# Performance work log

Measured on AMD Instinct MI355X. Metric: run time of the kernel, lower is better.

Reference implementation:

```python
import jax, jax.numpy as jnp
import numpy as np
from math import factorial, sqrt, pi

LMAX, NSH = 2, 9
F = 64
N_RBF = 20
N_INTER = 2
N_ATOMS = 1000
N_PAIRS = 10000
CUTOFF = 5.0

# ---------- Clebsch-Gordan coefficients for real spherical harmonics ----------

def _cg_complex(l1, m1, l2, m2, l3, m3):
    # <l1 m1 l2 m2 | l3 m3> via Racah formula
    if m3 != m1 + m2 or not (abs(l1 - l2) <= l3 <= l1 + l2):
        return 0.0
    f = factorial
    pre = sqrt((2 * l3 + 1) * f(l3 + l1 - l2) * f(l3 - l1 + l2) * f(l1 + l2 - l3) / f(l1 + l2 + l3 + 1))
    pre *= sqrt(f(l3 + m3) * f(l3 - m3) * f(l1 - m1) * f(l1 + m1) * f(l2 - m2) * f(l2 + m2))
    s = 0.0
    for k in range(l1 + l2 - l3 + 1):
        d = [k, l1 + l2 - l3 - k, l1 - m1 - k, l2 + m2 - k, l3 - l2 + m1 + k, l3 - l1 - m2 + k]
        if min(d) < 0:
            continue
        s += (-1) ** k / np.prod([float(f(t)) for t in d])
    return pre * s

def _sh_indices(lmax):
    l = np.concatenate([np.full(2 * ll + 1, ll) for ll in range(lmax + 1)])
    m = np.concatenate([np.arange(-ll, ll + 1) for ll in range(lmax + 1)])
    return l, m

def _real_cg(lmax):
    lidx, midx = _sh_indices(lmax)
    n = (lmax + 1) ** 2
    cgc = np.zeros((n, n, n))
    for a in range(n):
        for b in range(n):
            for c in range(n):
                cgc[a, b, c] = _cg_complex(lidx[a], midx[a], lidx[b], midx[b], lidx[c], midx[c])
    # complex -> real spherical harmonic change of basis (per degree l)
    U = np.zeros((n, n), dtype=np.complex128)
    for ll in range(lmax + 1):
        base = ll * ll + ll
        U[base, base] = 1.0
        for m in range(1, ll + 1):
            U[base + m, base - m] = 1 / sqrt(2)
            U[base + m, base + m] = (-1) ** m / sqrt(2)
            U[base - m, base - m] = 1j / sqrt(2)
            U[base - m, base + m] = -1j * (-1) ** m / sqrt(2)
    cgr = np.einsum('ijk,ai,bj,ck->abc', cgc.astype(np.complex128), U, U, U.conj())
    parity = (-1.0) ** lidx
    mask = (parity[:, None, None] * parity[None, :, None]) == parity[None, None, :]
    cgr = np.real(cgr) * mask
    cgr = np.transpose(cgr, (2, 0, 1))  # [s_out, s_in(x), s_filter(Y)]
    s1, s2, s3 = np.nonzero(np.abs(cgr) > 1e-9)
    return s1, s2, s3, cgr[s1, s2, s3].astype(np.float32), lidx

_S1, _S2, _S3, _CGV, _LIDX = _real_cg(LMAX)
IDX1 = jnp.asarray(_S1)            # output sh channel per CG path
IDX2 = jnp.asarray(_S2)            # input-feature sh channel per CG path
IDX3 = jnp.asarray(_S3)            # Ylm sh channel per CG path
CGVAL = jnp.asarray(_CGV)          # CG value per path
WIDX = jnp.asarray(_LIDX[_S3])     # radial-filter degree per CG path
LIDX = jnp.asarray(_LIDX)          # degree of each of the 9 sh channels

# ---------- real spherical harmonics (lmax=2, orthonormal, m=-l..l order) ----------

def _rsh(u):
    x, y, z = u[:, 0], u[:, 1], u[:, 2]
    c1 = sqrt(3.0 / (4.0 * pi))
    c2 = 0.5 * sqrt(15.0 / pi)
    return jnp.stack([
        jnp.full_like(x, 0.5 / sqrt(pi)),
        c1 * y, c1 * z, c1 * x,
        c2 * x * y,
        c2 * y * z,
        0.25 * sqrt(5.0 / pi) * (3.0 * z * z - 1.0),
        c2 * x * z,
        0.25 * sqrt(15.0 / pi) * (x * x - y * y),
    ], axis=1)


def setup_inputs() -> dict:
    key = jax.random.key(0)
    ks = jax.random.split(key, 10)
    atomic_numbers = jax.random.randint(ks[0], (N_ATOMS,), 0, 100)
    r_ij = 1.5 * jax.random.normal(ks[1], (N_PAIRS, 3), dtype=jnp.float32)
    idx_i = jnp.sort(jax.random.randint(ks[2], (N_PAIRS,), 0, N_ATOMS))
    idx_j = jax.random.randint(ks[3], (N_PAIRS,), 0, N_ATOMS)
    emb = jax.random.normal(ks[4], (100, F), dtype=jnp.float32)
    def s(k, sh, fan):
        return jax.random.normal(k, sh, dtype=jnp.float32) / float(np.sqrt(fan))
    Wf = s(ks[5], (N_INTER, N_RBF, (LMAX + 1) * F), N_RBF)
    bf = jnp.zeros((N_INTER, (LMAX + 1) * F), jnp.float32)
    W1 = s(ks[6], (N_INTER, F, F), F)
    W2 = s(ks[7], (N_INTER, F, F), F)
    W3 = s(ks[8], (N_INTER, F, F), F)
    Wg = s(ks[9], (N_INTER, F, (LMAX + 1) * F), F)
    bg = jnp.zeros((N_INTER, (LMAX + 1) * F), jnp.float32)
    return dict(atomic_numbers=atomic_numbers, r_ij=r_ij, idx_i=idx_i, idx_j=idx_j,
                emb=emb, Wf=Wf, bf=bf, W1=W1, W2=W2, W3=W3, Wg=Wg, bg=bg)


def reference(atomic_numbers, r_ij, idx_i, idx_j, emb, Wf, bf, W1, W2, W3, Wg, bg):
    n_atoms = atomic_numbers.shape[0]
    d = jnp.linalg.norm(r_ij, axis=1, keepdims=True)          # [P,1]
    Yij = _rsh(r_ij / d)                                       # [P,9]
    offsets = jnp.linspace(0.0, CUTOFF, N_RBF)                 # GaussianRBF
    width = CUTOFF / (N_RBF - 1)
    radial = jnp.exp((-0.5 / (width * width)) * (d - offsets) ** 2)   # [P,n_rbf]
    cut = 0.5 * (jnp.cos(d * (pi / CUTOFF)) + 1.0) * (d < CUTOFF)     # [P,1]
    # nuclear embedding + scalar2rsh (zero-pad l>0 channels)
    x = jnp.zeros((n_atoms, NSH, F), emb.dtype).at[:, 0, :].set(emb[atomic_numbers])
    for t in range(N_INTER):
        # SO3Convolution
        Wij = (radial @ Wf[t] + bf[t]).reshape(-1, LMAX + 1, F) * cut[:, :, None]  # [P,lmax+1,F]
        xj = x[idx_j]                                                              # [P,9,F]
        v = xj[:, IDX2] * Yij[:, IDX3, None] * Wij[:, WIDX] * CGVAL[None, :, None]  # [P,nnz,F]
        yij = jnp.zeros_like(xj).at[:, IDX1].add(v)                                 # CG scatter
        dx = jax.ops.segment_sum(yij, idx_i, num_segments=n_atoms)                  # edge->node scatter
        # mixing1 + SO3TensorProduct
        ddx = dx @ W1[t]
        tp = jnp.zeros_like(dx).at[:, IDX1].add(dx[:, IDX2] * ddx[:, IDX3] * CGVAL[None, :, None])
        dx = (dx + tp) @ W2[t]
        # SO3ParametricGatedNonlinearity (gate from l=0 channel)
        gate = (dx[:, 0] @ Wg[t] + bg[t]).reshape(-1, LMAX + 1, F)
        dx = dx * jax.nn.sigmoid(gate[:, LIDX])
        dx = dx @ W3[t]
        x = x + dx
    return x  # multipole_representation [n_atoms, 9, F]; x[:,0] is scalar_representation
```

## Files before the change

kernel.cpp:

```cpp
#include <hip/hip_runtime.h>
#include <cmath>

constexpr int kNsh    = 9;
constexpr int kF      = 64;
constexpr int kNrbf   = 20;
constexpr int kNAtoms = 1000;
constexpr int kNPairs = 10000;
constexpr float kCutoffF = 5.0f;
constexpr int kMaxNZ  = 200;
constexpr int kCp     = 12;
constexpr int kXs     = kF * kCp;

struct CGSparse {
  int n;
  int c[kMaxNZ];
  int a[kMaxNZ];
  int b[kMaxNZ];
  float v[kMaxNZ];
};

constexpr double cfact(int n) {
  double r = 1.0;
  for (int i = 2; i <= n; i++) r *= (double)i;
  return r;
}
constexpr double cabs_(double x) { return x < 0 ? -x : x; }
constexpr double csqrt_(double x) {
  if (x <= 0.0) return 0.0;
  double g = x < 1.0 ? 1.0 : x;
  for (int i = 0; i < 60; i++) g = 0.5 * (g + x / g);
  return g;
}

constexpr double cg_cplx(int l1, int m1, int l2, int m2, int l3, int m3) {
  if (m3 != m1 + m2) return 0.0;
  int lo = l1 > l2 ? l1 - l2 : l2 - l1;
  if (l3 < lo || l3 > l1 + l2) return 0.0;
  double pre = csqrt_((2 * l3 + 1) * cfact(l3 + l1 - l2) * cfact(l3 - l1 + l2) *
                      cfact(l1 + l2 - l3) / cfact(l1 + l2 + l3 + 1));
  pre *= csqrt_(cfact(l3 + m3) * cfact(l3 - m3) * cfact(l1 - m1) *
                cfact(l1 + m1) * cfact(l2 - m2) * cfact(l2 + m2));
  double s = 0.0;
  for (int k = 0; k <= l1 + l2 - l3; k++) {
    int d0 = k, d1 = l1 + l2 - l3 - k, d2 = l1 - m1 - k;
    int d3 = l2 + m2 - k, d4 = l3 - l2 + m1 + k, d5 = l3 - l1 - m2 + k;
    if (d0 < 0 || d1 < 0 || d2 < 0 || d3 < 0 || d4 < 0 || d5 < 0) continue;
    double den = cfact(d0) * cfact(d1) * cfact(d2) * cfact(d3) * cfact(d4) * cfact(d5);
    s += ((k % 2) ? -1.0 : 1.0) / den;
  }
  return pre * s;
}

constexpr CGSparse build_cg() {
  CGSparse out{};
  int lidx[9] = {0, 1, 1, 1, 2, 2, 2, 2, 2};
  int midx[9] = {0, -1, 0, 1, -2, -1, 0, 1, 2};
  double Ur[9][9] = {};
  double Ui[9][9] = {};
  for (int l = 0; l <= 2; l++) {
    int base = l * l + l;
    Ur[base][base] = 1.0;
    for (int m = 1; m <= l; m++) {
      double s2 = 1.0 / csqrt_(2.0);
      double sgn = (m % 2) ? -1.0 : 1.0;
      Ur[base + m][base - m] = s2;
      Ur[base + m][base + m] = sgn * s2;
      Ui[base - m][base - m] = s2;
      Ui[base - m][base + m] = -sgn * s2;
    }
  }
  double cgr[9][9][9] = {};
  for (int i = 0; i < 9; i++)
    for (int j = 0; j < 9; j++)
      for (int k = 0; k < 9; k++) {
        double cv = cg_cplx(lidx[i], midx[i], lidx[j], midx[j], lidx[k], midx[k]);
        if (cv == 0.0) continue;
        for (int a2 = 0; a2 < 9; a2++) {
          if (Ur[a2][i] == 0.0 && Ui[a2][i] == 0.0) continue;
          for (int b2 = 0; b2 < 9; b2++) {
            if (Ur[b2][j] == 0.0 && Ui[b2][j] == 0.0) continue;
            for (int c2 = 0; c2 < 9; c2++) {
              if (Ur[c2][k] == 0.0 && Ui[c2][k] == 0.0) continue;
              double ar = Ur[a2][i], ai = Ui[a2][i];
              double br = Ur[b2][j], bi = Ui[b2][j];
              double cr = Ur[c2][k], ci = -Ui[c2][k];
              double pr = ar * br - ai * bi;
              double pi = ar * bi + ai * br;
              double rr = pr * cr - pi * ci;
              cgr[c2][a2][b2] += rr * cv;
            }
          }
        }
      }
  int n = 0;
  for (int c2 = 0; c2 < 9; c2++)
    for (int a2 = 0; a2 < 9; a2++)
      for (int b2 = 0; b2 < 9; b2++) {
        bool mask = ((lidx[a2] + lidx[b2]) % 2) == (lidx[c2] % 2);
        double v = mask ? cgr[c2][a2][b2] : 0.0;
        if (cabs_(v) > 1e-9) {
          out.c[n] = c2;
          out.a[n] = a2;
          out.b[n] = b2;
          out.v[n] = (float)v;
          n++;
        }
      }
  out.n = n;
  return out;
}

constexpr CGSparse CG = build_cg();
static_assert(CG.n > 0 && CG.n <= kMaxNZ, "CG table size out of range");

constexpr int kPreBlkPairs = kNPairs / 4;
constexpr int kPreBlkSeg   = (kNAtoms + 1 + 255) / 256;
constexpr int kPreBlkTotal = kPreBlkPairs + kPreBlkSeg;

__global__ __launch_bounds__(256) void k_pre(
    const float* __restrict__ rij, const float* __restrict__ Wf,
    const float* __restrict__ bf, const int* __restrict__ idx_i,
    float* __restrict__ Ypd, float* __restrict__ Wpair,
    int* __restrict__ seg) {
  const int blk = blockIdx.x;
  if (blk < kPreBlkPairs) {
    int wv = threadIdx.x >> 6;
    int f = threadIdx.x & 63;
    int p = blk * 4 + wv;
    float rx = rij[3 * p + 0], ry = rij[3 * p + 1], rz = rij[3 * p + 2];
    float d = sqrtf(rx * rx + ry * ry + rz * rz);
    float inv = 1.0f / d;
    float x = rx * inv, y = ry * inv, z = rz * inv;
    const float c0 = 0.28209479177387814f;
    const float c1 = 0.4886025119029199f;
    const float c2 = 1.0925484305920792f;
    const float c3 = 0.31539156525252005f;
    const float c4 = 0.5462742152960396f;
    if (f < 9) {
      float yv =
          (f == 0) ? c0 :
          (f == 1) ? c1 * y :
          (f == 2) ? c1 * z :
          (f == 3) ? c1 * x :
          (f == 4) ? c2 * x * y :
          (f == 5) ? c2 * y * z :
          (f == 6) ? c3 * (3.0f * z * z - 1.0f) :
          (f == 7) ? c2 * x * z :
                     c4 * (x * x - y * y);
      Ypd[p * 16 + f] = yv;
    }
    float cut = (d < kCutoffF) ? 0.5f * (cosf(d * (float)(M_PI / 5.0)) + 1.0f) : 0.0f;
    float radial[kNrbf];
    const float width = kCutoffF / (kNrbf - 1);
    const float coef = -0.5f / (width * width);
    #pragma unroll
    for (int k = 0; k < kNrbf; k++) {
      float off = (kCutoffF * k) / (kNrbf - 1);
      float tt = d - off;
      radial[k] = expf(coef * tt * tt);
    }
    #pragma unroll
    for (int t = 0; t < 2; t++) {
      #pragma unroll
      for (int l = 0; l < 3; l++) {
        float w = bf[t * 192 + l * 64 + f];
        #pragma unroll
        for (int k = 0; k < kNrbf; k++) {
          w += radial[k] * Wf[t * (kNrbf * 192) + k * 192 + l * 64 + f];
        }
        Wpair[t * (kNPairs * 192) + p * 192 + l * 64 + f] = w * cut;
      }
    }
  } else {
    int a = (blk - kPreBlkPairs) * 256 + threadIdx.x;
    if (a <= kNAtoms) {
      int lo = 0, hi = kNPairs;
      while (lo < hi) {
        int mid = (lo + hi) >> 1;
        if (idx_i[mid] < a) lo = mid + 1; else hi = mid;
      }
      seg[a] = lo;
    }
  }
}

__device__ __forceinline__ void stage_w(const float* __restrict__ W,
                                        float* __restrict__ sW, int tid) {
  const float4* g4 = (const float4*)W;
  float4* s4 = (float4*)sW;
  #pragma unroll
  for (int r = 0; r < 4; r++) s4[r * 256 + tid] = g4[r * 256 + tid];
}

__device__ __forceinline__ void mm_phase(const float* __restrict__ sA,
                                         const float* __restrict__ sW,
                                         float* __restrict__ sRw,
                                         int k0, int cgi, int fb) {
  if (cgi >= 3) return;
  const int c0 = cgi * 4;
  float acc[4][4];
  #pragma unroll
  for (int i = 0; i < 4; i++)
    #pragma unroll
    for (int j = 0; j < 4; j++) acc[i][j] = 0.f;
  #pragma unroll 4
  for (int kk = 0; kk < 16; kk++) {
    int k = k0 + kk;
    float4 av = *(const float4*)(sA + k * kCp + c0);
    float4 wv = *(const float4*)(sW + k * kF + fb);
    float a[4] = {av.x, av.y, av.z, av.w};
    float w[4] = {wv.x, wv.y, wv.z, wv.w};
    #pragma unroll
    for (int i = 0; i < 4; i++)
      #pragma unroll
      for (int j = 0; j < 4; j++) acc[i][j] += a[i] * w[j];
  }
  #pragma unroll
  for (int j = 0; j < 4; j++) {
    float4 v = {acc[0][j], acc[1][j], acc[2][j], acc[3][j]};
    *(float4*)(sRw + (fb + j) * kCp + c0) = v;
  }
}

template <int T>
__global__ __launch_bounds__(256) void k_inter(
    const float* __restrict__ Ypd, const float* __restrict__ Wpt,
    const int* __restrict__ seg, const int* __restrict__ idx_j,
    const int* __restrict__ Z, const float* __restrict__ emb,
    const float* __restrict__ x_in, const float* __restrict__ W1,
    const float* __restrict__ W2, const float* __restrict__ W3,
    const float* __restrict__ Wg, const float* __restrict__ bg,
    float* __restrict__ x_out) {
  const int atom = blockIdx.x;
  const int tid = threadIdx.x;
  const int wv = tid >> 6;
  const int lane = tid & 63;
  const int cgi = lane >> 4;
  const int fb = (lane & 15) * 4;
  const int k0 = wv * 16;

  __shared__ __align__(16) float sA[kF * kCp];
  __shared__ __align__(16) float sW[kF * kF];
  __shared__ __align__(16) float sR[4][kF * kCp];
  __shared__ __align__(16) float sGp[4][192];

  stage_w(W1, sW, tid);

  {
    float y[12];
    #pragma unroll
    for (int c = 0; c < 12; c++) y[c] = 0.f;
    const int s0 = seg[atom], s1 = seg[atom + 1];
    for (int p0 = s0 + wv; p0 < s1; p0 += 4) {
      const int p = __builtin_amdgcn_readfirstlane(p0);
      const int j = __builtin_amdgcn_readfirstlane(idx_j[p]);
      const float* Wp = Wpt + p * 192;
      float Wl0 = Wp[lane], Wl1 = Wp[64 + lane], Wl2 = Wp[128 + lane];
      const float* Yp = Ypd + p * 16;
      float YW[9];
      YW[0] = Yp[0] * Wl0;
      YW[1] = Yp[1] * Wl1;
      YW[2] = Yp[2] * Wl1;
      YW[3] = Yp[3] * Wl1;
      #pragma unroll
      for (int b = 4; b < 9; b++) YW[b] = Yp[b] * Wl2;
      if (T == 0) {
        float e = emb[Z[j] * kF + lane];
        #pragma unroll
        for (int q = 0; q < CG.n; q++) {
          if (CG.a[q] == 0) y[CG.c[q]] += CG.v[q] * YW[CG.b[q]] * e;
        }
      } else {
        const float* xj = x_in + j * kXs + lane * kCp;
        float xv[12];
        *(float4*)&xv[0] = *(const float4*)(xj + 0);
        *(float4*)&xv[4] = *(const float4*)(xj + 4);
        *(float4*)&xv[8] = *(const float4*)(xj + 8);
        #pragma unroll
        for (int q = 0; q < CG.n; q++) {
          y[CG.c[q]] += CG.v[q] * YW[CG.b[q]] * xv[CG.a[q]];
        }
      }
    }
    float4* r4 = (float4*)(sR[wv] + lane * kCp);
    r4[0] = *(float4*)&y[0];
    r4[1] = *(float4*)&y[4];
    r4[2] = *(float4*)&y[8];
  }
  __syncthreads();
  {
    const int i = tid * 3;
    #pragma unroll
    for (int d = 0; d < 3; d++) {
      sA[i + d] = sR[0][i + d] + sR[1][i + d] + sR[2][i + d] + sR[3][i + d];
    }
  }
  __syncthreads();

  mm_phase(sA, sW, sR[wv], k0, cgi, fb);
  __syncthreads();

  stage_w(W2, sW, tid);
  if (wv == 0) {
    float dxv[12], ddx[12];
    {
      const float4* sa = (const float4*)(sA + lane * kCp);
      *(float4*)&dxv[0] = sa[0];
      *(float4*)&dxv[4] = sa[1];
      *(float4*)&dxv[8] = sa[2];
    }
    #pragma unroll
    for (int c = 0; c < 12; c++) {
      ddx[c] = sR[0][lane * kCp + c] + sR[1][lane * kCp + c] +
               sR[2][lane * kCp + c] + sR[3][lane * kCp + c];
    }
    float t2[12];
    #pragma unroll
    for (int c = 0; c < 9; c++) t2[c] = dxv[c];
    t2[9] = 0.f; t2[10] = 0.f; t2[11] = 0.f;
    #pragma unroll
    for (int q = 0; q < CG.n; q++) {
      t2[CG.c[q]] += CG.v[q] * dxv[CG.a[q]] * ddx[CG.b[q]];
    }
    float4* sa = (float4*)(sA + lane * kCp);
    sa[0] = *(float4*)&t2[0];
    sa[1] = *(float4*)&t2[4];
    sa[2] = *(float4*)&t2[8];
  }
  __syncthreads();

  mm_phase(sA, sW, sR[wv], k0, cgi, fb);
  __syncthreads();

  stage_w(W3, sW, tid);
  {
    float g0 = 0.f, g1 = 0.f, g2 = 0.f;
    #pragma unroll 4
    for (int kk = 0; kk < 16; kk++) {
      int k = k0 + kk;
      float a = sR[0][k * kCp] + sR[1][k * kCp] + sR[2][k * kCp] + sR[3][k * kCp];
      g0 += a * Wg[k * 192 + lane];
      g1 += a * Wg[k * 192 + 64 + lane];
      g2 += a * Wg[k * 192 + 128 + lane];
    }
    sGp[wv][lane] = g0;
    sGp[wv][64 + lane] = g1;
    sGp[wv][128 + lane] = g2;
  }
  __syncthreads();

  if (wv == 0) {
    float dx2v[12];
    #pragma unroll
    for (int c = 0; c < 12; c++) {
      dx2v[c] = sR[0][lane * kCp + c] + sR[1][lane * kCp + c] +
                sR[2][lane * kCp + c] + sR[3][lane * kCp + c];
    }
    float g0 = bg[lane] + sGp[0][lane] + sGp[1][lane] + sGp[2][lane] + sGp[3][lane];
    float g1 = bg[64 + lane] + sGp[0][64 + lane] + sGp[1][64 + lane] +
               sGp[2][64 + lane] + sGp[3][64 + lane];
    float g2 = bg[128 + lane] + sGp[0][128 + lane] + sGp[1][128 + lane] +
               sGp[2][128 + lane] + sGp[3][128 + lane];
    g0 = 1.f / (1.f + expf(-g0));
    g1 = 1.f / (1.f + expf(-g1));
    g2 = 1.f / (1.f + expf(-g2));
    float dx3[12];
    dx3[0] = dx2v[0] * g0;
    dx3[1] = dx2v[1] * g1;
    dx3[2] = dx2v[2] * g1;
    dx3[3] = dx2v[3] * g1;
    #pragma unroll
    for (int c = 4; c < 9; c++) dx3[c] = dx2v[c] * g2;
    dx3[9] = 0.f; dx3[10] = 0.f; dx3[11] = 0.f;
    float4* sa = (float4*)(sA + lane * kCp);
    sa[0] = *(float4*)&dx3[0];
    sa[1] = *(float4*)&dx3[4];
    sa[2] = *(float4*)&dx3[8];
  }
  __syncthreads();

  mm_phase(sA, sW, sR[wv], k0, cgi, fb);
  __syncthreads();

  if (T == 0) {
    const int zi = Z[atom];
    const int i = tid * 3;
    #pragma unroll
    for (int d = 0; d < 3; d++) {
      const int idx = i + d;
      const int c = idx % kCp;
      float v = sR[0][idx] + sR[1][idx] + sR[2][idx] + sR[3][idx];
      if (c == 0) v += emb[zi * kF + idx / kCp];
      x_out[atom * kXs + idx] = v;
    }
  } else {
    for (int i = tid; i < kNsh * kF; i += 256) {
      int c = i >> 6, f = i & 63;
      int o = f * kCp + c;
      float v = sR[0][o] + sR[1][o] + sR[2][o] + sR[3][o] +
                x_in[atom * kXs + o];
      x_out[atom * (kNsh * kF) + i] = v;
    }
  }
}

extern "C" void kernel_launch(void* const* d_in, const int* in_sizes, int n_in,
                              void* d_out, int out_size, void* d_ws, size_t ws_size,
                              hipStream_t stream) {
  const int* Z        = (const int*)d_in[0];
  const float* rij    = (const float*)d_in[1];
  const int* idx_i    = (const int*)d_in[2];
  const int* idx_j    = (const int*)d_in[3];
  const float* emb    = (const float*)d_in[4];
  const float* Wf     = (const float*)d_in[5];
  const float* bf     = (const float*)d_in[6];
  const float* W1     = (const float*)d_in[7];
  const float* W2     = (const float*)d_in[8];
  const float* W3     = (const float*)d_in[9];
  const float* Wg     = (const float*)d_in[10];
  const float* bg     = (const float*)d_in[11];
  float* out = (float*)d_out;

  float* x1    = (float*)d_ws;
  float* Ypd   = x1 + kNAtoms * kXs;
  float* Wpair = Ypd + kNPairs * 16;
  int*   seg   = (int*)(Wpair + 2 * kNPairs * 192);

  k_pre<<<kPreBlkTotal, 256, 0, stream>>>(rij, Wf, bf, idx_i, Ypd, Wpair, seg);

  k_inter<0><<<kNAtoms, 256, 0, stream>>>(
      Ypd, Wpair, seg, idx_j, Z, emb, x1,
      W1, W2, W3, Wg, bg, x1);

  k_inter<1><<<kNAtoms, 256, 0, stream>>>(
      Ypd, Wpair + kNPairs * 192, seg, idx_j, Z, emb, x1,
      W1 + kF * kF, W2 + kF * kF, W3 + kF * kF,
      Wg + kF * 192, bg + 192, out);
}
```

Measured before the change: 126.6 us.

## Fuse per-pair radial/SH precompute into interaction kernels and keep weights in registers

Removes the k_pre kernel that materialized per-pair Y and filter weights in global memory. Each interaction kernel now recomputes the spherical harmonics, cutoff and radial filter inline per pair, and a tiny k_seg kernel computes the segment offsets. Mixing weights move from shared-memory staging into per-thread float4 registers, prefetched before the barriers. The reductions and output stores are vectorized with float4. This trades global write/read traffic and a launch for repeated radial-filter math (20 exps plus a 60-term dot product per pair per layer) and higher register pressure.

```diff
diff --git a/kernel.cpp b/kernel.cpp
--- a/kernel.cpp
+++ b/kernel.cpp
@@ -113,87 +113,30 @@
 constexpr CGSparse CG = build_cg();
 static_assert(CG.n > 0 && CG.n <= kMaxNZ, "CG table size out of range");
 
-constexpr int kPreBlkPairs = kNPairs / 4;
-constexpr int kPreBlkSeg   = (kNAtoms + 1 + 255) / 256;
-constexpr int kPreBlkTotal = kPreBlkPairs + kPreBlkSeg;
-
-__global__ __launch_bounds__(256) void k_pre(
-    const float* __restrict__ rij, const float* __restrict__ Wf,
-    const float* __restrict__ bf, const int* __restrict__ idx_i,
-    float* __restrict__ Ypd, float* __restrict__ Wpair,
-    int* __restrict__ seg) {
-  const int blk = blockIdx.x;
-  if (blk < kPreBlkPairs) {
-    int wv = threadIdx.x >> 6;
-    int f = threadIdx.x & 63;
-    int p = blk * 4 + wv;
-    float rx = rij[3 * p + 0], ry = rij[3 * p + 1], rz = rij[3 * p + 2];
-    float d = sqrtf(rx * rx + ry * ry + rz * rz);
-    float inv = 1.0f / d;
-    float x = rx * inv, y = ry * inv, z = rz * inv;
-    const float c0 = 0.28209479177387814f;
-    const float c1 = 0.4886025119029199f;
-    const float c2 = 1.0925484305920792f;
-    const float c3 = 0.31539156525252005f;
-    const float c4 = 0.5462742152960396f;
-    if (f < 9) {
-      float yv =
-          (f == 0) ? c0 :
-          (f == 1) ? c1 * y :
-          (f == 2) ? c1 * z :
-          (f == 3) ? c1 * x :
-          (f == 4) ? c2 * x * y :
-          (f == 5) ? c2 * y * z :
-          (f == 6) ? c3 * (3.0f * z * z - 1.0f) :
-          (f == 7) ? c2 * x * z :
-                     c4 * (x * x - y * y);
-      Ypd[p * 16 + f] = yv;
-    }
-    float cut = (d < kCutoffF) ? 0.5f * (cosf(d * (float)(M_PI / 5.0)) + 1.0f) : 0.0f;
-    float radial[kNrbf];
-    const float width = kCutoffF / (kNrbf - 1);
-    const float coef = -0.5f / (width * width);
-    #pragma unroll
-    for (int k = 0; k < kNrbf; k++) {
-      float off = (kCutoffF * k) / (kNrbf - 1);
-      float tt = d - off;
-      radial[k] = expf(coef * tt * tt);
-    }
-    #pragma unroll
-    for (int t = 0; t < 2; t++) {
-      #pragma unroll
-      for (int l = 0; l < 3; l++) {
-        float w = bf[t * 192 + l * 64 + f];
-        #pragma unroll
-        for (int k = 0; k < kNrbf; k++) {
-          w += radial[k] * Wf[t * (kNrbf * 192) + k * 192 + l * 64 + f];
-        }
-        Wpair[t * (kNPairs * 192) + p * 192 + l * 64 + f] = w * cut;
-      }
-    }
-  } else {
-    int a = (blk - kPreBlkPairs) * 256 + threadIdx.x;
-    if (a <= kNAtoms) {
-      int lo = 0, hi = kNPairs;
-      while (lo < hi) {
-        int mid = (lo + hi) >> 1;
-        if (idx_i[mid] < a) lo = mid + 1; else hi = mid;
-      }
-      seg[a] = lo;
-    }
-  }
-}
-
-__device__ __forceinline__ void stage_w(const float* __restrict__ W,
-                                        float* __restrict__ sW, int tid) {
-  const float4* g4 = (const float4*)W;
-  float4* s4 = (float4*)sW;
+__global__ __launch_bounds__(64) void k_seg(const int* __restrict__ idx_i,
+                                            int* __restrict__ seg) {
+  int a = blockIdx.x * 64 + threadIdx.x;
+  if (a <= kNAtoms) {
+    int lo = 0, hi = kNPairs;
+    while (lo < hi) {
+      int mid = (lo + hi) >> 1;
+      if (idx_i[mid] < a) lo = mid + 1; else hi = mid;
+    }
+    seg[a] = lo;
+  }
+}
+
+__device__ __forceinline__ void load_w(const float* __restrict__ W,
+                                       float4* __restrict__ wr,
+                                       int k0, int fb) {
   #pragma unroll
-  for (int r = 0; r < 4; r++) s4[r * 256 + tid] = g4[r * 256 + tid];
+  for (int kk = 0; kk < 16; kk++) {
+    wr[kk] = *(const float4*)(W + (k0 + kk) * kF + fb);
+  }
 }
 
 __device__ __forceinline__ void mm_phase(const float* __restrict__ sA,
-                                         const float* __restrict__ sW,
+                                         const float4* __restrict__ wr,
                                          float* __restrict__ sRw,
                                          int k0, int cgi, int fb) {
   if (cgi >= 3) return;
@@ -203,11 +146,11 @@
   for (int i = 0; i < 4; i++)
     #pragma unroll
     for (int j = 0; j < 4; j++) acc[i][j] = 0.f;
-  #pragma unroll 4
+  #pragma unroll
   for (int kk = 0; kk < 16; kk++) {
     int k = k0 + kk;
     float4 av = *(const float4*)(sA + k * kCp + c0);
-    float4 wv = *(const float4*)(sW + k * kF + fb);
+    float4 wv = wr[kk];
     float a[4] = {av.x, av.y, av.z, av.w};
     float w[4] = {wv.x, wv.y, wv.z, wv.w};
     #pragma unroll
@@ -224,13 +167,13 @@
 
 template <int T>
 __global__ __launch_bounds__(256) void k_inter(
-    const float* __restrict__ Ypd, const float* __restrict__ Wpt,
-    const int* __restrict__ seg, const int* __restrict__ idx_j,
-    const int* __restrict__ Z, const float* __restrict__ emb,
-    const float* __restrict__ x_in, const float* __restrict__ W1,
-    const float* __restrict__ W2, const float* __restrict__ W3,
-    const float* __restrict__ Wg, const float* __restrict__ bg,
-    float* __restrict__ x_out) {
+    const float* __restrict__ rij, const float* __restrict__ Wf,
+    const float* __restrict__ bf, const int* __restrict__ seg,
+    const int* __restrict__ idx_j, const int* __restrict__ Z,
+    const float* __restrict__ emb, const float* __restrict__ x_in,
+    const float* __restrict__ W1, const float* __restrict__ W2,
+    const float* __restrict__ W3, const float* __restrict__ Wg,
+    const float* __restrict__ bg, float* __restrict__ x_out) {
   const int atom = blockIdx.x;
   const int tid = threadIdx.x;
   const int wv = tid >> 6;
@@ -240,11 +183,8 @@
   const int k0 = wv * 16;
 
   __shared__ __align__(16) float sA[kF * kCp];
-  __shared__ __align__(16) float sW[kF * kF];
   __shared__ __align__(16) float sR[4][kF * kCp];
   __shared__ __align__(16) float sGp[4][192];
-
-  stage_w(W1, sW, tid);
 
   {
     float y[12];
@@ -253,17 +193,54 @@
     const int s0 = seg[atom], s1 = seg[atom + 1];
     for (int p0 = s0 + wv; p0 < s1; p0 += 4) {
       const int p = __builtin_amdgcn_readfirstlane(p0);
+      float rx = rij[3 * p + 0], ry = rij[3 * p + 1], rz = rij[3 * p + 2];
+      float d = sqrtf(rx * rx + ry * ry + rz * rz);
+      float inv = 1.0f / d;
+      float ux = rx * inv, uy = ry * inv, uz = rz * inv;
+      const float c0 = 0.28209479177387814f;
+      const float c1 = 0.4886025119029199f;
+      const float c2 = 1.0925484305920792f;
+      const float c3 = 0.31539156525252005f;
+      const float c4 = 0.5462742152960396f;
+      float Y[9];
+      Y[0] = c0;
+      Y[1] = c1 * uy;
+      Y[2] = c1 * uz;
+      Y[3] = c1 * ux;
+      Y[4] = c2 * ux * uy;
+      Y[5] = c2 * uy * uz;
+      Y[6] = c3 * (3.0f * uz * uz - 1.0f);
+      Y[7] = c2 * ux * uz;
+      Y[8] = c4 * (ux * ux - uy * uy);
+      float cut = (d < kCutoffF)
+                      ? 0.5f * (cosf(d * (float)(M_PI / 5.0)) + 1.0f) : 0.0f;
+      float radial[kNrbf];
+      const float width = kCutoffF / (kNrbf - 1);
+      const float coef = -0.5f / (width * width);
+      #pragma unroll
+      for (int k = 0; k < kNrbf; k++) {
+        float off = (kCutoffF * k) / (kNrbf - 1);
+        float tt = d - off;
+        radial[k] = expf(coef * tt * tt);
+      }
+      float Wl[3];
+      #pragma unroll
+      for (int l = 0; l < 3; l++) {
+        float w = bf[l * 64 + lane];
+        #pragma unroll
+        for (int k = 0; k < kNrbf; k++) {
+          w += radial[k] * Wf[k * 192 + l * 64 + lane];
+        }
+        Wl[l] = w * cut;
+      }
+      float YW[9];
+      YW[0] = Y[0] * Wl[0];
+      YW[1] = Y[1] * Wl[1];
+      YW[2] = Y[2] * Wl[1];
+      YW[3] = Y[3] * Wl[1];
+      #pragma unroll
+      for (int b = 4; b < 9; b++) YW[b] = Y[b] * Wl[2];
       const int j = __builtin_amdgcn_readfirstlane(idx_j[p]);
-      const float* Wp = Wpt + p * 192;
-      float Wl0 = Wp[lane], Wl1 = Wp[64 + lane], Wl2 = Wp[128 + lane];
-      const float* Yp = Ypd + p * 16;
-      float YW[9];
-      YW[0] = Yp[0] * Wl0;
-      YW[1] = Yp[1] * Wl1;
-      YW[2] = Yp[2] * Wl1;
-      YW[3] = Yp[3] * Wl1;
-      #pragma unroll
-      for (int b = 4; b < 9; b++) YW[b] = Yp[b] * Wl2;
       if (T == 0) {
         float e = emb[Z[j] * kF + lane];
         #pragma unroll
@@ -287,20 +264,25 @@
     r4[1] = *(float4*)&y[4];
     r4[2] = *(float4*)&y[8];
   }
-  __syncthreads();
-  {
-    const int i = tid * 3;
-    #pragma unroll
-    for (int d = 0; d < 3; d++) {
-      sA[i + d] = sR[0][i + d] + sR[1][i + d] + sR[2][i + d] + sR[3][i + d];
-    }
-  }
-  __syncthreads();
-
-  mm_phase(sA, sW, sR[wv], k0, cgi, fb);
-  __syncthreads();
-
-  stage_w(W2, sW, tid);
+  float4 wr[16];
+  load_w(W1, wr, k0, fb);
+  __syncthreads();
+  if (tid < 192) {
+    const float4* r0 = (const float4*)sR[0];
+    const float4* r1 = (const float4*)sR[1];
+    const float4* r2 = (const float4*)sR[2];
+    const float4* r3 = (const float4*)sR[3];
+    float4 a = r0[tid], b = r1[tid], c = r2[tid], d = r3[tid];
+    float4 s = {a.x + b.x + c.x + d.x, a.y + b.y + c.y + d.y,
+                a.z + b.z + c.z + d.z, a.w + b.w + c.w + d.w};
+    ((float4*)sA)[tid] = s;
+  }
+  __syncthreads();
+
+  mm_phase(sA, wr, sR[wv], k0, cgi, fb);
+  load_w(W2, wr, k0, fb);
+  __syncthreads();
+
   if (wv == 0) {
     float dxv[12], ddx[12];
     {
@@ -329,10 +311,10 @@
   }
   __syncthreads();
 
-  mm_phase(sA, sW, sR[wv], k0, cgi, fb);
-  __syncthreads();
-
-  stage_w(W3, sW, tid);
+  mm_phase(sA, wr, sR[wv], k0, cgi, fb);
+  load_w(W3, wr, k0, fb);
+  __syncthreads();
+
   {
     float g0 = 0.f, g1 = 0.f, g2 = 0.f;
     #pragma unroll 4
@@ -379,27 +361,42 @@
   }
   __syncthreads();
 
-  mm_phase(sA, sW, sR[wv], k0, cgi, fb);
+  mm_phase(sA, wr, sR[wv], k0, cgi, fb);
   __syncthreads();
 
   if (T == 0) {
-    const int zi = Z[atom];
-    const int i = tid * 3;
-    #pragma unroll
-    for (int d = 0; d < 3; d++) {
-      const int idx = i + d;
-      const int c = idx % kCp;
-      float v = sR[0][idx] + sR[1][idx] + sR[2][idx] + sR[3][idx];
-      if (c == 0) v += emb[zi * kF + idx / kCp];
-      x_out[atom * kXs + idx] = v;
+    if (tid < 192) {
+      const int f = tid / 3, r = tid % 3;
+      const float4* r0 = (const float4*)sR[0];
+      const float4* r1 = (const float4*)sR[1];
+      const float4* r2 = (const float4*)sR[2];
+      const float4* r3 = (const float4*)sR[3];
+      float4 a = r0[tid], b = r1[tid], c = r2[tid], d = r3[tid];
+      float4 s = {a.x + b.x + c.x + d.x, a.y + b.y + c.y + d.y,
+                  a.z + b.z + c.z + d.z, a.w + b.w + c.w + d.w};
+      if (r == 0) s.x += emb[Z[atom] * kF + f];
+      *(float4*)(x_out + atom * kXs + tid * 4) = s;
     }
   } else {
-    for (int i = tid; i < kNsh * kF; i += 256) {
-      int c = i >> 6, f = i & 63;
-      int o = f * kCp + c;
-      float v = sR[0][o] + sR[1][o] + sR[2][o] + sR[3][o] +
-                x_in[atom * kXs + o];
-      x_out[atom * (kNsh * kF) + i] = v;
+    if (tid < 192) {
+      const float4* r0 = (const float4*)sR[0];
+      const float4* r1 = (const float4*)sR[1];
+      const float4* r2 = (const float4*)sR[2];
+      const float4* r3 = (const float4*)sR[3];
+      float4 a = r0[tid], b = r1[tid], c = r2[tid], d = r3[tid];
+      float4 xi = *(const float4*)(x_in + atom * kXs + tid * 4);
+      float4 s = {a.x + b.x + c.x + d.x + xi.x, a.y + b.y + c.y + d.y + xi.y,
+                  a.z + b.z + c.z + d.z + xi.z, a.w + b.w + c.w + d.w + xi.w};
+      ((float4*)sA)[tid] = s;
+    }
+    __syncthreads();
+    #pragma unroll
+    for (int r = 0; r < 3; r++) {
+      int i = r * 256 + tid;
+      if (i < kNsh * kF) {
+        int c = i >> 6, f = i & 63;
+        x_out[atom * (kNsh * kF) + i] = sA[f * kCp + c];
+      }
     }
   }
 }
@@ -421,19 +418,17 @@
   const float* bg     = (const float*)d_in[11];
   float* out = (float*)d_out;
 
-  float* x1    = (float*)d_ws;
-  float* Ypd   = x1 + kNAtoms * kXs;
-  float* Wpair = Ypd + kNPairs * 16;
-  int*   seg   = (int*)(Wpair + 2 * kNPairs * 192);
-
-  k_pre<<<kPreBlkTotal, 256, 0, stream>>>(rij, Wf, bf, idx_i, Ypd, Wpair, seg);
+  float* x1  = (float*)d_ws;
+  int*   seg = (int*)(x1 + kNAtoms * kXs);
+
+  k_seg<<<16, 64, 0, stream>>>(idx_i, seg);
 
   k_inter<0><<<kNAtoms, 256, 0, stream>>>(
-      Ypd, Wpair, seg, idx_j, Z, emb, x1,
+      rij, Wf, bf, seg, idx_j, Z, emb, x1,
       W1, W2, W3, Wg, bg, x1);
 
   k_inter<1><<<kNAtoms, 256, 0, stream>>>(
-      Ypd, Wpair + kNPairs * 192, seg, idx_j, Z, emb, x1,
+      rij, Wf + kNrbf * 192, bf + 192, seg, idx_j, Z, emb, x1,
       W1 + kF * kF, W2 + kF * kF, W3 + kF * kF,
       Wg + kF * 192, bg + 192, out);
 }
```

Measured after the change: 136.1 us. 1.07x slower.

## Use single-wavefront blocks per atom and read weights directly from global

Applied to the files above, without the earlier changes.

The interaction kernel now runs one 64-thread wavefront per atom instead of four wavefronts. Each thread owns one feature and loops over all of the atom's pairs, loading neighbor indices in batches of 64 and broadcasting them with shuffles. The 64x64 matmuls read W1/W2/W3 straight from global/L2 instead of staging them in shared memory. This removes the cross-wave partial-sum reductions, most barriers, and the shared-memory weight staging, and it cuts LDS use per block. The cost is that each atom's pair loop is now serialized on one wave, with less latency hiding per atom and more global weight traffic.

```diff
diff --git a/kernel.cpp b/kernel.cpp
--- a/kernel.cpp
+++ b/kernel.cpp
@@ -184,46 +184,38 @@
   }
 }
 
-__device__ __forceinline__ void stage_w(const float* __restrict__ W,
-                                        float* __restrict__ sW, int tid) {
-  const float4* g4 = (const float4*)W;
-  float4* s4 = (float4*)sW;
-  #pragma unroll
-  for (int r = 0; r < 4; r++) s4[r * 256 + tid] = g4[r * 256 + tid];
-}
-
-__device__ __forceinline__ void mm_phase(const float* __restrict__ sA,
-                                         const float* __restrict__ sW,
-                                         float* __restrict__ sRw,
-                                         int k0, int cgi, int fb) {
-  if (cgi >= 3) return;
-  const int c0 = cgi * 4;
-  float acc[4][4];
-  #pragma unroll
-  for (int i = 0; i < 4; i++)
-    #pragma unroll
-    for (int j = 0; j < 4; j++) acc[i][j] = 0.f;
-  #pragma unroll 4
-  for (int kk = 0; kk < 16; kk++) {
-    int k = k0 + kk;
-    float4 av = *(const float4*)(sA + k * kCp + c0);
-    float4 wv = *(const float4*)(sW + k * kF + fb);
-    float a[4] = {av.x, av.y, av.z, av.w};
-    float w[4] = {wv.x, wv.y, wv.z, wv.w};
+__device__ __forceinline__ void mm64(const float* __restrict__ sA,
+                                     const float* __restrict__ W,
+                                     float* __restrict__ sB,
+                                     int cgi, int fb) {
+  if (cgi < 3) {
+    const int c0 = cgi * 4;
+    float acc[4][4];
     #pragma unroll
     for (int i = 0; i < 4; i++)
       #pragma unroll
-      for (int j = 0; j < 4; j++) acc[i][j] += a[i] * w[j];
-  }
-  #pragma unroll
-  for (int j = 0; j < 4; j++) {
-    float4 v = {acc[0][j], acc[1][j], acc[2][j], acc[3][j]};
-    *(float4*)(sRw + (fb + j) * kCp + c0) = v;
+      for (int j = 0; j < 4; j++) acc[i][j] = 0.f;
+    #pragma unroll 8
+    for (int k = 0; k < kF; k++) {
+      float4 av = *(const float4*)(sA + k * kCp + c0);
+      float4 wv = *(const float4*)(W + k * kF + fb);
+      float a[4] = {av.x, av.y, av.z, av.w};
+      float w[4] = {wv.x, wv.y, wv.z, wv.w};
+      #pragma unroll
+      for (int i = 0; i < 4; i++)
+        #pragma unroll
+        for (int j = 0; j < 4; j++) acc[i][j] += a[i] * w[j];
+    }
+    #pragma unroll
+    for (int j = 0; j < 4; j++) {
+      float4 v = {acc[0][j], acc[1][j], acc[2][j], acc[3][j]};
+      *(float4*)(sB + (fb + j) * kCp + c0) = v;
+    }
   }
 }
 
 template <int T>
-__global__ __launch_bounds__(256) void k_inter(
+__global__ __launch_bounds__(64) void k_inter(
     const float* __restrict__ Ypd, const float* __restrict__ Wpt,
     const int* __restrict__ seg, const int* __restrict__ idx_j,
     const int* __restrict__ Z, const float* __restrict__ emb,
@@ -232,88 +224,74 @@
     const float* __restrict__ Wg, const float* __restrict__ bg,
     float* __restrict__ x_out) {
   const int atom = blockIdx.x;
-  const int tid = threadIdx.x;
-  const int wv = tid >> 6;
-  const int lane = tid & 63;
-  const int cgi = lane >> 4;
-  const int fb = (lane & 15) * 4;
-  const int k0 = wv * 16;
-
-  __shared__ __align__(16) float sA[kF * kCp];
-  __shared__ __align__(16) float sW[kF * kF];
-  __shared__ __align__(16) float sR[4][kF * kCp];
-  __shared__ __align__(16) float sGp[4][192];
-
-  stage_w(W1, sW, tid);
-
+  const int f = threadIdx.x;
+  const int cgi = f >> 4;
+  const int fb = (f & 15) * 4;
+
+  __shared__ __align__(16) float sA[kF * kCp + 4];
+  __shared__ __align__(16) float sB[kF * kCp + 4];
+
+  float dxv[12];
+  #pragma unroll
+  for (int c = 0; c < 12; c++) dxv[c] = 0.f;
   {
-    float y[12];
-    #pragma unroll
-    for (int c = 0; c < 12; c++) y[c] = 0.f;
     const int s0 = seg[atom], s1 = seg[atom + 1];
-    for (int p0 = s0 + wv; p0 < s1; p0 += 4) {
-      const int p = __builtin_amdgcn_readfirstlane(p0);
-      const int j = __builtin_amdgcn_readfirstlane(idx_j[p]);
-      const float* Wp = Wpt + p * 192;
-      float Wl0 = Wp[lane], Wl1 = Wp[64 + lane], Wl2 = Wp[128 + lane];
-      const float* Yp = Ypd + p * 16;
-      float YW[9];
-      YW[0] = Yp[0] * Wl0;
-      YW[1] = Yp[1] * Wl1;
-      YW[2] = Yp[2] * Wl1;
-      YW[3] = Yp[3] * Wl1;
-      #pragma unroll
-      for (int b = 4; b < 9; b++) YW[b] = Yp[b] * Wl2;
-      if (T == 0) {
-        float e = emb[Z[j] * kF + lane];
+    for (int base = s0; base < s1; base += 64) {
+      const int n = min(64, s1 - base);
+      int jv = 0, zv = 0;
+      if (f < n) jv = idx_j[base + f];
+      if (T == 0) zv = (f < n) ? Z[jv] : 0;
+      for (int it = 0; it < n; it++) {
+        const int p = base + it;
+        const float* Wp = Wpt + p * 192;
+        float Wl0 = Wp[f], Wl1 = Wp[64 + f], Wl2 = Wp[128 + f];
+        const float* Yp = Ypd + p * 16;
+        float YW[9];
+        YW[0] = Yp[0] * Wl0;
+        YW[1] = Yp[1] * Wl1;
+        YW[2] = Yp[2] * Wl1;
+        YW[3] = Yp[3] * Wl1;
         #pragma unroll
-        for (int q = 0; q < CG.n; q++) {
-          if (CG.a[q] == 0) y[CG.c[q]] += CG.v[q] * YW[CG.b[q]] * e;
-        }
-      } else {
-        const float* xj = x_in + j * kXs + lane * kCp;
-        float xv[12];
-        *(float4*)&xv[0] = *(const float4*)(xj + 0);
-        *(float4*)&xv[4] = *(const float4*)(xj + 4);
-        *(float4*)&xv[8] = *(const float4*)(xj + 8);
-        #pragma unroll
-        for (int q = 0; q < CG.n; q++) {
-          y[CG.c[q]] += CG.v[q] * YW[CG.b[q]] * xv[CG.a[q]];
+        for (int b = 4; b < 9; b++) YW[b] = Yp[b] * Wl2;
+        if (T == 0) {
+          const int z = __shfl(zv, it, 64);
+          float e = emb[z * kF + f];
+          #pragma unroll
+          for (int q = 0; q < CG.n; q++) {
+            if (CG.a[q] == 0) dxv[CG.c[q]] += CG.v[q] * YW[CG.b[q]] * e;
+          }
+        } else {
+          const int j = __shfl(jv, it, 64);
+          const float* xj = x_in + j * kXs + f * kCp;
+          float xv[12];
+          *(float4*)&xv[0] = *(const float4*)(xj + 0);
+          *(float4*)&xv[4] = *(const float4*)(xj + 4);
+          *(float4*)&xv[8] = *(const float4*)(xj + 8);
+          #pragma unroll
+          for (int q = 0; q < CG.n; q++) {
+            dxv[CG.c[q]] += CG.v[q] * YW[CG.b[q]] * xv[CG.a[q]];
+          }
         }
       }
     }
-    float4* r4 = (float4*)(sR[wv] + lane * kCp);
-    r4[0] = *(float4*)&y[0];
-    r4[1] = *(float4*)&y[4];
-    r4[2] = *(float4*)&y[8];
-  }
-  __syncthreads();
+  }
   {
-    const int i = tid * 3;
-    #pragma unroll
-    for (int d = 0; d < 3; d++) {
-      sA[i + d] = sR[0][i + d] + sR[1][i + d] + sR[2][i + d] + sR[3][i + d];
-    }
-  }
-  __syncthreads();
-
-  mm_phase(sA, sW, sR[wv], k0, cgi, fb);
-  __syncthreads();
-
-  stage_w(W2, sW, tid);
-  if (wv == 0) {
-    float dxv[12], ddx[12];
-    {
-      const float4* sa = (const float4*)(sA + lane * kCp);
-      *(float4*)&dxv[0] = sa[0];
-      *(float4*)&dxv[4] = sa[1];
-      *(float4*)&dxv[8] = sa[2];
-    }
-    #pragma unroll
-    for (int c = 0; c < 12; c++) {
-      ddx[c] = sR[0][lane * kCp + c] + sR[1][lane * kCp + c] +
-               sR[2][lane * kCp + c] + sR[3][lane * kCp + c];
-    }
+    float4* sa = (float4*)(sA + f * kCp);
+    sa[0] = *(float4*)&dxv[0];
+    sa[1] = *(float4*)&dxv[4];
+    sa[2] = *(float4*)&dxv[8];
+  }
+  __syncthreads();
+
+  mm64(sA, W1, sB, cgi, fb);
+  __syncthreads();
+
+  {
+    float ddx[12];
+    const float4* sb = (const float4*)(sB + f * kCp);
+    *(float4*)&ddx[0] = sb[0];
+    *(float4*)&ddx[4] = sb[1];
+    *(float4*)&ddx[8] = sb[2];
     float t2[12];
     #pragma unroll
     for (int c = 0; c < 9; c++) t2[c] = dxv[c];
@@ -322,48 +300,33 @@
     for (int q = 0; q < CG.n; q++) {
       t2[CG.c[q]] += CG.v[q] * dxv[CG.a[q]] * ddx[CG.b[q]];
     }
-    float4* sa = (float4*)(sA + lane * kCp);
+    float4* sa = (float4*)(sA + f * kCp);
     sa[0] = *(float4*)&t2[0];
     sa[1] = *(float4*)&t2[4];
     sa[2] = *(float4*)&t2[8];
   }
   __syncthreads();
 
-  mm_phase(sA, sW, sR[wv], k0, cgi, fb);
-  __syncthreads();
-
-  stage_w(W3, sW, tid);
+  mm64(sA, W2, sB, cgi, fb);
+  __syncthreads();
+
   {
-    float g0 = 0.f, g1 = 0.f, g2 = 0.f;
+    float g0 = bg[f], g1 = bg[64 + f], g2 = bg[128 + f];
     #pragma unroll 4
-    for (int kk = 0; kk < 16; kk++) {
-      int k = k0 + kk;
-      float a = sR[0][k * kCp] + sR[1][k * kCp] + sR[2][k * kCp] + sR[3][k * kCp];
-      g0 += a * Wg[k * 192 + lane];
-      g1 += a * Wg[k * 192 + 64 + lane];
-      g2 += a * Wg[k * 192 + 128 + lane];
-    }
-    sGp[wv][lane] = g0;
-    sGp[wv][64 + lane] = g1;
-    sGp[wv][128 + lane] = g2;
-  }
-  __syncthreads();
-
-  if (wv == 0) {
-    float dx2v[12];
-    #pragma unroll
-    for (int c = 0; c < 12; c++) {
-      dx2v[c] = sR[0][lane * kCp + c] + sR[1][lane * kCp + c] +
-                sR[2][lane * kCp + c] + sR[3][lane * kCp + c];
-    }
-    float g0 = bg[lane] + sGp[0][lane] + sGp[1][lane] + sGp[2][lane] + sGp[3][lane];
-    float g1 = bg[64 + lane] + sGp[0][64 + lane] + sGp[1][64 + lane] +
-               sGp[2][64 + lane] + sGp[3][64 + lane];
-    float g2 = bg[128 + lane] + sGp[0][128 + lane] + sGp[1][128 + lane] +
-               sGp[2][128 + lane] + sGp[3][128 + lane];
+    for (int k = 0; k < kF; k++) {
+      float a = sB[k * kCp];
+      g0 += a * Wg[k * 192 + f];
+      g1 += a * Wg[k * 192 + 64 + f];
+      g2 += a * Wg[k * 192 + 128 + f];
+    }
     g0 = 1.f / (1.f + expf(-g0));
     g1 = 1.f / (1.f + expf(-g1));
     g2 = 1.f / (1.f + expf(-g2));
+    float dx2v[12];
+    const float4* sb = (const float4*)(sB + f * kCp);
+    *(float4*)&dx2v[0] = sb[0];
+    *(float4*)&dx2v[4] = sb[1];
+    *(float4*)&dx2v[8] = sb[2];
     float dx3[12];
     dx3[0] = dx2v[0] * g0;
     dx3[1] = dx2v[1] * g1;
@@ -372,34 +335,39 @@
     #pragma unroll
     for (int c = 4; c < 9; c++) dx3[c] = dx2v[c] * g2;
     dx3[9] = 0.f; dx3[10] = 0.f; dx3[11] = 0.f;
-    float4* sa = (float4*)(sA + lane * kCp);
+    float4* sa = (float4*)(sA + f * kCp);
     sa[0] = *(float4*)&dx3[0];
     sa[1] = *(float4*)&dx3[4];
     sa[2] = *(float4*)&dx3[8];
   }
   __syncthreads();
 
-  mm_phase(sA, sW, sR[wv], k0, cgi, fb);
+  mm64(sA, W3, sB, cgi, fb);
   __syncthreads();
 
   if (T == 0) {
-    const int zi = Z[atom];
-    const int i = tid * 3;
-    #pragma unroll
-    for (int d = 0; d < 3; d++) {
-      const int idx = i + d;
-      const int c = idx % kCp;
-      float v = sR[0][idx] + sR[1][idx] + sR[2][idx] + sR[3][idx];
-      if (c == 0) v += emb[zi * kF + idx / kCp];
-      x_out[atom * kXs + idx] = v;
-    }
+    float o[12];
+    const float4* sb = (const float4*)(sB + f * kCp);
+    *(float4*)&o[0] = sb[0];
+    *(float4*)&o[4] = sb[1];
+    *(float4*)&o[8] = sb[2];
+    o[0] += emb[Z[atom] * kF + f];
+    float4* xo = (float4*)(x_out + atom * kXs + f * kCp);
+    xo[0] = *(float4*)&o[0];
+    xo[1] = *(float4*)&o[4];
+    xo[2] = *(float4*)&o[8];
   } else {
-    for (int i = tid; i < kNsh * kF; i += 256) {
-      int c = i >> 6, f = i & 63;
-      int o = f * kCp + c;
-      float v = sR[0][o] + sR[1][o] + sR[2][o] + sR[3][o] +
-                x_in[atom * kXs + o];
-      x_out[atom * (kNsh * kF) + i] = v;
+    float o[12];
+    const float4* sb = (const float4*)(sB + f * kCp);
+    const float4* xi = (const float4*)(x_in + atom * kXs + f * kCp);
+    float4 a0 = sb[0], a1 = sb[1], a2 = sb[2];
+    float4 b0 = xi[0], b1 = xi[1], b2 = xi[2];
+    o[0] = a0.x + b0.x; o[1] = a0.y + b0.y; o[2] = a0.z + b0.z; o[3] = a0.w + b0.w;
+    o[4] = a1.x + b1.x; o[5] = a1.y + b1.y; o[6] = a1.z + b1.z; o[7] = a1.w + b1.w;
+    o[8] = a2.x + b2.x;
+    #pragma unroll
+    for (int c = 0; c < 9; c++) {
+      x_out[atom * (kNsh * kF) + c * kF + f] = o[c];
     }
   }
 }
@@ -428,11 +396,11 @@
 
   k_pre<<<kPreBlkTotal, 256, 0, stream>>>(rij, Wf, bf, idx_i, Ypd, Wpair, seg);
 
-  k_inter<0><<<kNAtoms, 256, 0, stream>>>(
+  k_inter<0><<<kNAtoms, 64, 0, stream>>>(
       Ypd, Wpair, seg, idx_j, Z, emb, x1,
       W1, W2, W3, Wg, bg, x1);
 
-  k_inter<1><<<kNAtoms, 256, 0, stream>>>(
+  k_inter<1><<<kNAtoms, 64, 0, stream>>>(
       Ypd, Wpair + kNPairs * 192, seg, idx_j, Z, emb, x1,
       W1 + kF * kF, W2 + kF * kF, W3 + kF * kF,
       Wg + kF * 192, bg + 192, out);
```

Result: slower. 141.7 us (+11.9%).
